# Optimization experiments

Hardware: AMD Instinct MI355X
Metric: run time of the kernel (lower is better)

## Reference

```python
import jax, jax.numpy as jnp
from jax import lax
import numpy as np

PATCH_H = 8
PATCH_W = 8


def setup_inputs() -> dict:
    key = jax.random.key(0)
    k1, k2 = jax.random.split(key)
    x = jax.random.normal(k1, (2, 1024, 256, 256), dtype=jnp.float32)
    # Conv1d weight [C_out, C_in, k], bias=False
    conv_w = jax.random.normal(k2, (1024, 1024, 3), dtype=jnp.float32) * 0.02
    return {"x": x, "conv_w": conv_w}


def reference(x, conv_w):
    B, C, H, W = x.shape
    hf, wf = H // PATCH_H, W // PATCH_W
    P = hf * wf
    # Patch average pool: mean over each (PATCH_H, PATCH_W) tile -> [B, C, hf, wf]
    xp = x.reshape(B, C, hf, PATCH_H, wf, PATCH_W)
    y = xp.mean(axis=(3, 5)).reshape(B, C, P)
    # Conv1d over the patch axis (SAME padding, no bias), then sigmoid gate
    g = lax.conv_general_dilated(
        y, conv_w, window_strides=(1,), padding="SAME",
        dimension_numbers=("NCH", "OIH", "NCH"))
    g = jax.nn.sigmoid(g).reshape(B, C, hf, wf)
    # Broadcast gate back over each patch and multiply
    out = xp * g[:, :, :, None, :, None]
    return out.reshape(B, C, H, W)
```

## Files before the change

### kernel.cpp

```cpp
#include <hip/hip_runtime.h>
#include <hip/hip_bf16.h>

#define HH 256
#define WW 256
#define CCH 1024
#define NB 2
#define HF 32
#define WF 32
#define PP 1024

using f32x4 = __attribute__((ext_vector_type(4))) float;
using short8 = __attribute__((ext_vector_type(8))) short;

__global__ __launch_bounds__(256) void pool_kernel(const float* __restrict__ x,
                                                   float* __restrict__ y) {
    int blk = blockIdx.x;
    int ph  = blk & 31;
    int bc  = blk >> 5;
    int t   = threadIdx.x;
    const float* xp = x + ((size_t)bc * HH + (size_t)ph * 8) * WW;
    int r    = t >> 6;
    int col4 = (t & 63) * 4;
    float s = 0.f;
#pragma unroll
    for (int it = 0; it < 2; ++it) {
        float4 v = *(const float4*)(xp + (size_t)(r + it * 4) * WW + col4);
        s += v.x + v.y + v.z + v.w;
    }
    __shared__ float red[256];
    red[t] = s;
    __syncthreads();
    if (t < 32) {
        float tot = 0.f;
#pragma unroll
        for (int r4 = 0; r4 < 4; ++r4)
            tot += red[r4 * 64 + 2 * t] + red[r4 * 64 + 2 * t + 1];
        y[(size_t)bc * PP + ph * WF + t] = tot * (1.f / 64.f);
    }
}

__global__ __launch_bounds__(256) void wconv_kernel(const float* __restrict__ w,
                                                    __hip_bfloat16* __restrict__ wT) {
    int tid = blockIdx.x * 256 + threadIdx.x;
    const float* p = w + (size_t)tid * 3;
    float a = p[0], b = p[1], c = p[2];
    wT[tid]               = __float2bfloat16(a);
    wT[(1u << 20) + tid]  = __float2bfloat16(b);
    wT[(2u << 20) + tid]  = __float2bfloat16(c);
}

__global__ __launch_bounds__(256) void pad_kernel(__hip_bfloat16* __restrict__ yT) {
    int tid = blockIdx.x * 256 + threadIdx.x;
    int b = tid >> 10, c = tid & 1023;
    __hip_bfloat16 z = __float2bfloat16(0.f);
    __hip_bfloat16* base = yT + (size_t)b * (PP + 2) * CCH;
    base[c] = z;
    base[(size_t)(PP + 1) * CCH + c] = z;
}

__global__ __launch_bounds__(256) void transpose_kernel(const float* __restrict__ y,
                                                        __hip_bfloat16* __restrict__ yT) {
    int b  = blockIdx.z;
    int c0 = blockIdx.x * 32;
    int p0 = blockIdx.y * 32;
    __shared__ float tile[32][33];
    int tx = threadIdx.x, ty = threadIdx.y;
    const float* yb = y + (size_t)b * CCH * PP;
#pragma unroll
    for (int rr = 0; rr < 4; ++rr)
        tile[ty + rr * 8][tx] = yb[(size_t)(c0 + ty + rr * 8) * PP + p0 + tx];
    __syncthreads();
    __hip_bfloat16* yTb = yT + (size_t)b * (PP + 2) * CCH;
#pragma unroll
    for (int rr = 0; rr < 4; ++rr)
        yTb[(size_t)(1 + p0 + ty + rr * 8) * CCH + c0 + tx] =
            __float2bfloat16(tile[tx][ty + rr * 8]);
}

__global__ __launch_bounds__(256) void conv_gemm_kernel(
        const __hip_bfloat16* __restrict__ wT,
        const __hip_bfloat16* __restrict__ yT,
        float* __restrict__ gate) {
    int lane = threadIdx.x & 63;
    int wid  = threadIdx.x >> 6;
    int wr = wid >> 1, wc = wid & 1;
    int l15 = lane & 15, lhi = lane >> 4;
    int co_base = blockIdx.x * 64 + wr * 32;
    int p_base  = blockIdx.y * 64 + wc * 32;
    int b = blockIdx.z;
    const __hip_bfloat16* yTb = yT + (size_t)b * (PP + 2) * CCH;

    f32x4 acc[2][2] = {};
    for (int tap = 0; tap < 3; ++tap) {
        const __hip_bfloat16* Ap = wT + (size_t)tap * (1u << 20)
                                 + (size_t)(co_base + l15) * CCH + lhi * 8;
        const __hip_bfloat16* Bp = yTb + (size_t)(p_base + l15 + tap) * CCH + lhi * 8;
        for (int ci0 = 0; ci0 < CCH; ci0 += 32) {
            short8 a0 = *(const short8*)(Ap + ci0);
            short8 a1 = *(const short8*)(Ap + ci0 + 16 * CCH);
            short8 b0 = *(const short8*)(Bp + ci0);
            short8 b1 = *(const short8*)(Bp + ci0 + 16 * CCH);
            acc[0][0] = __builtin_amdgcn_mfma_f32_16x16x32_bf16(a0, b0, acc[0][0], 0, 0, 0);
            acc[0][1] = __builtin_amdgcn_mfma_f32_16x16x32_bf16(a0, b1, acc[0][1], 0, 0, 0);
            acc[1][0] = __builtin_amdgcn_mfma_f32_16x16x32_bf16(a1, b0, acc[1][0], 0, 0, 0);
            acc[1][1] = __builtin_amdgcn_mfma_f32_16x16x32_bf16(a1, b1, acc[1][1], 0, 0, 0);
        }
    }
    float* gb = gate + (size_t)b * CCH * PP;
#pragma unroll
    for (int i16 = 0; i16 < 2; ++i16) {
#pragma unroll
        for (int j16 = 0; j16 < 2; ++j16) {
            int col  = p_base + j16 * 16 + l15;
            int row0 = co_base + i16 * 16 + lhi * 4;
#pragma unroll
            for (int r = 0; r < 4; ++r) {
                float v = acc[i16][j16][r];
                gb[(size_t)(row0 + r) * PP + col] = 1.f / (1.f + __expf(-v));
            }
        }
    }
}

__global__ __launch_bounds__(256) void apply_kernel(const float* __restrict__ x,
                                                    const float* __restrict__ gate,
                                                    float* __restrict__ out) {
    size_t i0 = (size_t)blockIdx.x * blockDim.x + threadIdx.x;
    size_t stride = (size_t)gridDim.x * blockDim.x;
    const size_t total4 = (size_t)1 << 25;
    for (size_t i4 = i0; i4 < total4; i4 += stride) {
        int w4 = (int)(i4 & 63);
        int h  = (int)((i4 >> 6) & 255);
        int c  = (int)((i4 >> 14) & 1023);
        int b  = (int)(i4 >> 24);
        int p  = (h >> 3) * 32 + (w4 >> 1);
        float g = gate[(((size_t)b * 1024 + c) << 10) + p];
        float4 v = ((const float4*)x)[i4];
        float4 o;
        o.x = v.x * g; o.y = v.y * g; o.z = v.z * g; o.w = v.w * g;
        ((float4*)out)[i4] = o;
    }
}

extern "C" void kernel_launch(void* const* d_in, const int* in_sizes, int n_in,
                              void* d_out, int out_size, void* d_ws, size_t ws_size,
                              hipStream_t stream) {
    const float* x = (const float*)d_in[0];
    const float* w = (const float*)d_in[1];
    float* out = (float*)d_out;

    char* ws = (char*)d_ws;
    float*          y    = (float*)(ws);
    __hip_bfloat16* yT   = (__hip_bfloat16*)(ws + 8388608);
    __hip_bfloat16* wT   = (__hip_bfloat16*)(ws + 12591104);
    float*          gate = (float*)(ws + 18882560);

    hipLaunchKernelGGL(pool_kernel,      dim3(65536),      dim3(256),    0, stream, x, y);
    hipLaunchKernelGGL(wconv_kernel,     dim3(4096),       dim3(256),    0, stream, w, wT);
    hipLaunchKernelGGL(pad_kernel,       dim3(8),          dim3(256),    0, stream, yT);
    hipLaunchKernelGGL(transpose_kernel, dim3(32, 32, 2),  dim3(32, 8),  0, stream, y, yT);
    hipLaunchKernelGGL(conv_gemm_kernel, dim3(16, 16, 2),  dim3(256),    0, stream, wT, yT, gate);
    hipLaunchKernelGGL(apply_kernel,     dim3(2048),       dim3(256),    0, stream, x, gate, out);
}
```

Before: 432.7 us.

## Use nontemporal loads/stores, fuse pad into weight convert, shrink GEMM warp tile

The pool and apply kernels now use nontemporal loads and stores on the large x/out streams, so they pollute the cache less. The zero-padding kernel is folded into the weight conversion kernel, saving one launch. The conv GEMM now gives each wave a 16x32 tile instead of 32x32 and doubles the grid to raise occupancy and parallelism. The cost is more redundant global loads of B across waves.

```diff
diff --git a/kernel.cpp b/kernel.cpp
--- a/kernel.cpp
+++ b/kernel.cpp
@@ -24,7 +24,8 @@
     float s = 0.f;
 #pragma unroll
     for (int it = 0; it < 2; ++it) {
-        float4 v = *(const float4*)(xp + (size_t)(r + it * 4) * WW + col4);
+        f32x4 v = __builtin_nontemporal_load(
+            (const f32x4*)(xp + (size_t)(r + it * 4) * WW + col4));
         s += v.x + v.y + v.z + v.w;
     }
     __shared__ float red[256];
@@ -39,23 +40,22 @@
     }
 }
 
-__global__ __launch_bounds__(256) void wconv_kernel(const float* __restrict__ w,
-                                                    __hip_bfloat16* __restrict__ wT) {
+__global__ __launch_bounds__(256) void wconv_pad_kernel(const float* __restrict__ w,
+                                                        __hip_bfloat16* __restrict__ wT,
+                                                        __hip_bfloat16* __restrict__ yT) {
     int tid = blockIdx.x * 256 + threadIdx.x;
     const float* p = w + (size_t)tid * 3;
     float a = p[0], b = p[1], c = p[2];
     wT[tid]               = __float2bfloat16(a);
     wT[(1u << 20) + tid]  = __float2bfloat16(b);
     wT[(2u << 20) + tid]  = __float2bfloat16(c);
-}
-
-__global__ __launch_bounds__(256) void pad_kernel(__hip_bfloat16* __restrict__ yT) {
-    int tid = blockIdx.x * 256 + threadIdx.x;
-    int b = tid >> 10, c = tid & 1023;
-    __hip_bfloat16 z = __float2bfloat16(0.f);
-    __hip_bfloat16* base = yT + (size_t)b * (PP + 2) * CCH;
-    base[c] = z;
-    base[(size_t)(PP + 1) * CCH + c] = z;
+    if (tid < 2 * CCH) {
+        int bb = tid >> 10, cc = tid & 1023;
+        __hip_bfloat16 z = __float2bfloat16(0.f);
+        __hip_bfloat16* base = yT + (size_t)bb * (PP + 2) * CCH;
+        base[cc] = z;
+        base[(size_t)(PP + 1) * CCH + cc] = z;
+    }
 }
 
 __global__ __launch_bounds__(256) void transpose_kernel(const float* __restrict__ y,
@@ -83,41 +83,35 @@
         float* __restrict__ gate) {
     int lane = threadIdx.x & 63;
     int wid  = threadIdx.x >> 6;
-    int wr = wid >> 1, wc = wid & 1;
     int l15 = lane & 15, lhi = lane >> 4;
-    int co_base = blockIdx.x * 64 + wr * 32;
-    int p_base  = blockIdx.y * 64 + wc * 32;
+    int co_base = blockIdx.x * 64 + wid * 16;
+    int p_base  = blockIdx.y * 32;
     int b = blockIdx.z;
     const __hip_bfloat16* yTb = yT + (size_t)b * (PP + 2) * CCH;
 
-    f32x4 acc[2][2] = {};
+    f32x4 acc[2] = {};
+#pragma unroll
     for (int tap = 0; tap < 3; ++tap) {
         const __hip_bfloat16* Ap = wT + (size_t)tap * (1u << 20)
                                  + (size_t)(co_base + l15) * CCH + lhi * 8;
         const __hip_bfloat16* Bp = yTb + (size_t)(p_base + l15 + tap) * CCH + lhi * 8;
         for (int ci0 = 0; ci0 < CCH; ci0 += 32) {
             short8 a0 = *(const short8*)(Ap + ci0);
-            short8 a1 = *(const short8*)(Ap + ci0 + 16 * CCH);
             short8 b0 = *(const short8*)(Bp + ci0);
             short8 b1 = *(const short8*)(Bp + ci0 + 16 * CCH);
-            acc[0][0] = __builtin_amdgcn_mfma_f32_16x16x32_bf16(a0, b0, acc[0][0], 0, 0, 0);
-            acc[0][1] = __builtin_amdgcn_mfma_f32_16x16x32_bf16(a0, b1, acc[0][1], 0, 0, 0);
-            acc[1][0] = __builtin_amdgcn_mfma_f32_16x16x32_bf16(a1, b0, acc[1][0], 0, 0, 0);
-            acc[1][1] = __builtin_amdgcn_mfma_f32_16x16x32_bf16(a1, b1, acc[1][1], 0, 0, 0);
+            acc[0] = __builtin_amdgcn_mfma_f32_16x16x32_bf16(a0, b0, acc[0], 0, 0, 0);
+            acc[1] = __builtin_amdgcn_mfma_f32_16x16x32_bf16(a0, b1, acc[1], 0, 0, 0);
         }
     }
     float* gb = gate + (size_t)b * CCH * PP;
 #pragma unroll
-    for (int i16 = 0; i16 < 2; ++i16) {
+    for (int j16 = 0; j16 < 2; ++j16) {
+        int col  = p_base + j16 * 16 + l15;
+        int row0 = co_base + lhi * 4;
 #pragma unroll
-        for (int j16 = 0; j16 < 2; ++j16) {
-            int col  = p_base + j16 * 16 + l15;
-            int row0 = co_base + i16 * 16 + lhi * 4;
-#pragma unroll
-            for (int r = 0; r < 4; ++r) {
-                float v = acc[i16][j16][r];
-                gb[(size_t)(row0 + r) * PP + col] = 1.f / (1.f + __expf(-v));
-            }
+        for (int r = 0; r < 4; ++r) {
+            float v = acc[j16][r];
+            gb[(size_t)(row0 + r) * PP + col] = 1.f / (1.f + __expf(-v));
         }
     }
 }
@@ -135,10 +129,9 @@
         int b  = (int)(i4 >> 24);
         int p  = (h >> 3) * 32 + (w4 >> 1);
         float g = gate[(((size_t)b * 1024 + c) << 10) + p];
-        float4 v = ((const float4*)x)[i4];
-        float4 o;
-        o.x = v.x * g; o.y = v.y * g; o.z = v.z * g; o.w = v.w * g;
-        ((float4*)out)[i4] = o;
+        f32x4 v = __builtin_nontemporal_load((const f32x4*)x + i4);
+        v *= g;
+        __builtin_nontemporal_store(v, (f32x4*)out + i4);
     }
 }
 
@@ -156,9 +149,8 @@
     float*          gate = (float*)(ws + 18882560);
 
     hipLaunchKernelGGL(pool_kernel,      dim3(65536),      dim3(256),    0, stream, x, y);
-    hipLaunchKernelGGL(wconv_kernel,     dim3(4096),       dim3(256),    0, stream, w, wT);
-    hipLaunchKernelGGL(pad_kernel,       dim3(8),          dim3(256),    0, stream, yT);
+    hipLaunchKernelGGL(wconv_pad_kernel, dim3(4096),       dim3(256),    0, stream, w, wT, yT);
     hipLaunchKernelGGL(transpose_kernel, dim3(32, 32, 2),  dim3(32, 8),  0, stream, y, yT);
-    hipLaunchKernelGGL(conv_gemm_kernel, dim3(16, 16, 2),  dim3(256),    0, stream, wT, yT, gate);
+    hipLaunchKernelGGL(conv_gemm_kernel, dim3(16, 32, 2),  dim3(256),    0, stream, wT, yT, gate);
     hipLaunchKernelGGL(apply_kernel,     dim3(2048),       dim3(256),    0, stream, x, gate, out);
 }
```

Measured after the change: 426.5 us. Within noise of the previous version (-1.4%).
